# Kernel tuning notes

Measured on AMD Instinct MI355X. Metric: run time of the kernel, lower is better.

The kernel has to match this reference:

```python
import jax, jax.numpy as jnp
import numpy as np

NUM_EXPERTS = 8
TOP_K = 2
D_MODEL = 1024
D_HID = 4096
BATCH, SEQ = 2, 2048


def setup_inputs() -> dict:
    key = jax.random.key(0)
    ks = jax.random.split(key, 5)
    s = 0.02  # param scale
    return {
        "x": jax.random.normal(ks[0], (BATCH, SEQ, D_MODEL), dtype=jnp.float32),
        "Wg": jax.random.normal(ks[1], (D_MODEL, NUM_EXPERTS), dtype=jnp.float32) * s,
        "bg": jnp.zeros((NUM_EXPERTS,), dtype=jnp.float32),
        "W0": jax.random.normal(ks[2], (NUM_EXPERTS, D_MODEL, D_HID), dtype=jnp.float32) * s,
        "b0": jnp.zeros((NUM_EXPERTS, D_HID), dtype=jnp.float32),
        "W1": jax.random.normal(ks[3], (NUM_EXPERTS, D_MODEL, D_HID), dtype=jnp.float32) * s,
        "b1": jnp.zeros((NUM_EXPERTS, D_HID), dtype=jnp.float32),
        "W2": jax.random.normal(ks[4], (NUM_EXPERTS, D_HID, D_MODEL), dtype=jnp.float32) * s,
        "b2": jnp.zeros((NUM_EXPERTS, D_MODEL), dtype=jnp.float32),
    }


def reference(x, Wg, bg, W0, b0, W1, b1, W2, b2):
    n, s, d = x.shape
    # --- routing ---
    gate_logits = x @ Wg + bg                      # [n, s, E]
    top_vals, top_idx = jax.lax.top_k(gate_logits, TOP_K)  # [n, s, K]
    w = jax.nn.softmax(top_vals, axis=-1)          # [n, s, K]
    # combine weights scattered back to dense [n, s, E]
    combine = jnp.sum(jax.nn.one_hot(top_idx, NUM_EXPERTS, dtype=x.dtype) * w[..., None], axis=-2)
    # --- dense expert compute (all experts on all tokens, masked combine) ---
    xf = x.reshape(n * s, d)                       # [T, d]
    h = jnp.einsum('td,edh->eth', xf, W0) + b0[:, None, :]   # [E, T, H]
    g = jax.nn.silu(jnp.einsum('td,edh->eth', xf, W1) + b1[:, None, :])
    y = jnp.einsum('eth,ehd->etd', h * g, W2) + b2[:, None, :]  # [E, T, d]
    out = jnp.einsum('te,etd->td', combine.reshape(n * s, NUM_EXPERTS), y)
    return out.reshape(n, s, d)
```

## Files before the change

### kernel.cpp

```cpp
#include <hip/hip_runtime.h>

#define NTOK 4096
#define DM 1024
#define DH 4096
#define NE 8

typedef __attribute__((ext_vector_type(8))) short bf16x8;
typedef __attribute__((ext_vector_type(4))) float f32x4;
typedef __attribute__((ext_vector_type(8))) unsigned short u16x8;

__device__ __forceinline__ ushort f2bf(float f) {
  union { float f; unsigned u; } v; v.f = f;
  unsigned r = v.u + 0x7fffu + ((v.u >> 16) & 1u);
  return (ushort)(r >> 16);
}

#define GL2LDS(g, l) __builtin_amdgcn_global_load_lds( \
    (__attribute__((address_space(1))) const void*)(g), \
    (__attribute__((address_space(3))) void*)(l), 16, 0, 0)

__global__ __launch_bounds__(256) void gate_kernel(
    const float* __restrict__ x, const float* __restrict__ Wg,
    const float* __restrict__ bg, int* __restrict__ tkE,
    float* __restrict__ tkW, int* __restrict__ gcnt)
{
  const int wave = threadIdx.x >> 6;
  const int lane = threadIdx.x & 63;
  const int t = blockIdx.x * 4 + wave;

  float acc[NE];
#pragma unroll
  for (int e = 0; e < NE; e++) acc[e] = 0.f;

  for (int i = 0; i < DM / 64; i++) {
    int d = i * 64 + lane;
    float xv = x[(long)t * DM + d];
#pragma unroll
    for (int e = 0; e < NE; e++) acc[e] += xv * Wg[d * NE + e];
  }
#pragma unroll
  for (int e = 0; e < NE; e++) {
#pragma unroll
    for (int off = 32; off; off >>= 1) acc[e] += __shfl_xor(acc[e], off, 64);
    acc[e] += bg[e];
  }
  int e0 = 0; float v0 = acc[0];
#pragma unroll
  for (int e = 1; e < NE; e++) if (acc[e] > v0) { v0 = acc[e]; e0 = e; }
  int e1 = -1; float v1 = -3.4e38f;
#pragma unroll
  for (int e = 0; e < NE; e++) if (e != e0 && acc[e] > v1) { v1 = acc[e]; e1 = e; }
  float w0 = 1.f / (1.f + __expf(v1 - v0));
  float w1 = 1.f - w0;
  if (lane == 0) {
    tkE[t] = e0 | (e1 << 8);
    tkW[2 * t] = w0;
    tkW[2 * t + 1] = w1;
    atomicAdd(&gcnt[e0], 1);
    atomicAdd(&gcnt[e1], 1);
  }
}

__global__ void scan_kernel(const int* __restrict__ gcnt, int* __restrict__ offs,
                            int* __restrict__ cursor)
{
  if (threadIdx.x == 0) {
    int o = 0;
    for (int e = 0; e < NE; e++) { offs[e] = o; o += gcnt[e]; cursor[e] = 0; }
    offs[NE] = o;
  }
}

__global__ __launch_bounds__(256) void build_kernel(
    const int* __restrict__ tkE, const float* __restrict__ tkW,
    const int* __restrict__ offs, int* __restrict__ cursor,
    int* __restrict__ rmeta, float* __restrict__ rw)
{
  int t = blockIdx.x * 256 + threadIdx.x;
  int ee = tkE[t];
#pragma unroll
  for (int k = 0; k < 2; k++) {
    int e = (k == 0) ? (ee & 0xff) : (ee >> 8);
    int pos = atomicAdd(&cursor[e], 1);
    int row = offs[e] + pos;
    rmeta[row] = t * 2 + k;
    rw[row] = tkW[t * 2 + k];
  }
}

__global__ __launch_bounds__(256) void gather_kernel(
    const float* __restrict__ x, const int* __restrict__ rmeta,
    ushort* __restrict__ xg)
{
  int row = blockIdx.x;
  int t = rmeta[row] >> 1;
  const float4* src = (const float4*)(x + (long)t * DM);
  float4 v = src[threadIdx.x];
  ushort4 o = { f2bf(v.x), f2bf(v.y), f2bf(v.z), f2bf(v.w) };
  *(ushort4*)(xg + (long)row * DM + threadIdx.x * 4) = o;
}

__global__ __launch_bounds__(256) void transpose_cvt(
    const float* __restrict__ src, ushort* __restrict__ dst,
    int R, int C, long srcE, long dstE)
{
  __shared__ __align__(16) float tile[64][68];
  const int e = blockIdx.z;
  const int r0 = blockIdx.y * 64;
  const int c0 = blockIdx.x * 64;
  const float* s = src + (long)e * srcE;
  ushort* d = dst + (long)e * dstE;
  const int tid = threadIdx.x;
  const int lr = tid >> 4;
  const int lc4 = tid & 15;
#pragma unroll
  for (int p = 0; p < 4; p++) {
    int r = p * 16 + lr;
    float4 v = *(const float4*)&s[(long)(r0 + r) * C + c0 + lc4 * 4];
    *(float4*)&tile[r][lc4 * 4] = v;
  }
  __syncthreads();
  const int oc = tid >> 2;
  const int seg = tid & 3;
  u16x8 o0, o1;
#pragma unroll
  for (int j = 0; j < 8; j++) {
    o0[j] = f2bf(tile[seg * 8 + j][oc]);
    o1[j] = f2bf(tile[32 + seg * 8 + j][oc]);
  }
  ushort* dp = &d[(long)(c0 + oc) * R + r0];
  *(u16x8*)(dp + seg * 8) = o0;
  *(u16x8*)(dp + 32 + seg * 8) = o1;
}

__global__ __launch_bounds__(512, 2) void gemm1_kernel(
    const ushort* __restrict__ xg, const ushort* __restrict__ Wt01,
    const float* __restrict__ b0, const float* __restrict__ b1,
    const int* __restrict__ offs, ushort* __restrict__ aout)
{
  const int flat = blockIdx.x;
  const int xcd = flat & 7;
  const int rest = flat >> 3;
  const int mt = rest & 7;
  const int g2 = rest >> 3;
  const int val = g2 * 8 + xcd;
  const int e = val >> 5;
  const int nt = val & 31;

  const int off_e = offs[e];
  const int cnt = offs[e + 1] - off_e;
  if (mt * 256 >= cnt) return;
  const int nbase = nt * 128;

  __shared__ ushort As[2 * 256 * 64];
  __shared__ ushort Bh[2 * 128 * 64];
  __shared__ ushort Bg[2 * 128 * 64];

  const int tid = threadIdx.x;
  const int lane = tid & 63;
  const int wave = tid >> 6;
  const int wm = wave & 3;
  const int wn = wave >> 2;

  const ushort* Ap = xg + (long)(off_e + mt * 256) * DM;
  const ushort* Bhp = Wt01 + (long)e * (2 * DH) * DM + (long)nbase * DM;
  const ushort* Bgp = Bhp + (long)DH * DM;

  f32x4 acc_h[4][4], acc_g[4][4];
#pragma unroll
  for (int i = 0; i < 4; i++)
#pragma unroll
    for (int j = 0; j < 4; j++) {
      acc_h[i][j] = (f32x4){0.f, 0.f, 0.f, 0.f};
      acc_g[i][j] = (f32x4){0.f, 0.f, 0.f, 0.f};
    }

  auto stage = [&](int cur, int k0) {
#pragma unroll
    for (int s = 0; s < 4; s++) {
      int loff = s * 8192 + tid * 16;
      int row = loff >> 7;
      int sg = ((loff >> 4) & 7) ^ (row & 7);
      GL2LDS(Ap + (long)row * DM + k0 + sg * 8, (char*)As + cur * 32768 + loff);
    }
#pragma unroll
    for (int s = 0; s < 2; s++) {
      int loff = s * 8192 + tid * 16;
      int row = loff >> 7;
      int sg = ((loff >> 4) & 7) ^ (row & 7);
      GL2LDS(Bhp + (long)row * DM + k0 + sg * 8, (char*)Bh + cur * 16384 + loff);
      GL2LDS(Bgp + (long)row * DM + k0 + sg * 8, (char*)Bg + cur * 16384 + loff);
    }
  };

  stage(0, 0);
  stage(1, 64);

  for (int t = 0; t < 16; t++) {
    const int cur = t & 1;
    if (t < 15) asm volatile("s_waitcnt vmcnt(8)" ::: "memory");
    else        asm volatile("s_waitcnt vmcnt(0)" ::: "memory");
    __builtin_amdgcn_s_barrier();
    asm volatile("" ::: "memory");

    const char* Ab  = (const char*)As + cur * 32768;
    const char* Bhb = (const char*)Bh + cur * 16384;
    const char* Bgb = (const char*)Bg + cur * 16384;

    bf16x8 af[4][2];
#pragma unroll
    for (int mi = 0; mi < 4; mi++)
#pragma unroll
      for (int ks = 0; ks < 2; ks++) {
        int row = wm * 64 + mi * 16 + (lane & 15);
        int seg = ks * 4 + (lane >> 4);
        af[mi][ks] = *(const bf16x8*)(Ab + row * 128 + ((seg ^ (row & 7)) << 4));
      }
#pragma unroll
    for (int j = 0; j < 4; j++) {
      bf16x8 bh[2], bg[2];
#pragma unroll
      for (int ks = 0; ks < 2; ks++) {
        int row = wn * 64 + j * 16 + (lane & 15);
        int seg = ks * 4 + (lane >> 4);
        int o = row * 128 + ((seg ^ (row & 7)) << 4);
        bh[ks] = *(const bf16x8*)(Bhb + o);
        bg[ks] = *(const bf16x8*)(Bgb + o);
      }
      __builtin_amdgcn_s_setprio(1);
#pragma unroll
      for (int mi = 0; mi < 4; mi++) {
        acc_h[mi][j] = __builtin_amdgcn_mfma_f32_16x16x32_bf16(af[mi][0], bh[0], acc_h[mi][j], 0, 0, 0);
        acc_h[mi][j] = __builtin_amdgcn_mfma_f32_16x16x32_bf16(af[mi][1], bh[1], acc_h[mi][j], 0, 0, 0);
        acc_g[mi][j] = __builtin_amdgcn_mfma_f32_16x16x32_bf16(af[mi][0], bg[0], acc_g[mi][j], 0, 0, 0);
        acc_g[mi][j] = __builtin_amdgcn_mfma_f32_16x16x32_bf16(af[mi][1], bg[1], acc_g[mi][j], 0, 0, 0);
      }
      __builtin_amdgcn_s_setprio(0);
      __builtin_amdgcn_s_barrier();
    }
    asm volatile("" ::: "memory");
    if (t + 2 < 16) stage(cur, (t + 2) * 64);
  }

#pragma unroll
  for (int j = 0; j < 4; j++) {
    const int col = nbase + wn * 64 + j * 16 + (lane & 15);
    const float bb0 = b0[e * DH + col];
    const float bb1 = b1[e * DH + col];
#pragma unroll
    for (int mi = 0; mi < 4; mi++) {
#pragma unroll
      for (int r = 0; r < 4; r++) {
        int mlocal = mt * 256 + wm * 64 + mi * 16 + (lane >> 4) * 4 + r;
        if (mlocal < cnt) {
          float h = acc_h[mi][j][r] + bb0;
          float g = acc_g[mi][j][r] + bb1;
          float a = h * (g / (1.f + __expf(-g)));
          aout[(long)(off_e + mlocal) * DH + col] = f2bf(a);
        }
      }
    }
  }
}

__global__ __launch_bounds__(512, 2) void gemm2_kernel(
    const ushort* __restrict__ aout, const ushort* __restrict__ W2t,
    const int* __restrict__ offs, const int* __restrict__ rmeta,
    const float* __restrict__ rw, float* __restrict__ ybuf)
{
  const int flat = blockIdx.x;
  const int xcd = flat & 7;
  const int rest = flat >> 3;
  const int mt = rest & 7;
  const int g2 = rest >> 3;
  const int val = g2 * 8 + xcd;
  const int e = val >> 3;
  const int r2 = val & 7;
  const int nt = r2 >> 1;
  const int kc = r2 & 1;

  const int off_e = offs[e];
  const int cnt = offs[e + 1] - off_e;
  if (mt * 256 >= cnt) return;
  const int nbase = nt * 256;
  const int kbase = kc * 2048;

  __shared__ ushort As[2 * 256 * 64];
  __shared__ ushort Bs[2 * 256 * 64];

  const int tid = threadIdx.x;
  const int lane = tid & 63;
  const int wave = tid >> 6;
  const int wm = wave & 1;
  const int wn = wave >> 1;

  const ushort* Ap = aout + (long)(off_e + mt * 256) * DH;
  const ushort* Bp = W2t + (long)e * DM * DH + (long)nbase * DH;

  f32x4 acc[8][4];
#pragma unroll
  for (int i = 0; i < 8; i++)
#pragma unroll
    for (int j = 0; j < 4; j++) acc[i][j] = (f32x4){0.f, 0.f, 0.f, 0.f};

  auto stage = [&](int cur, int k0) {
#pragma unroll
    for (int s = 0; s < 4; s++) {
      int loff = s * 8192 + tid * 16;
      int row = loff >> 7;
      int sg = ((loff >> 4) & 7) ^ (row & 7);
      long gelem = (long)row * DH + k0 + sg * 8;
      GL2LDS(Ap + gelem, (char*)As + cur * 32768 + loff);
      GL2LDS(Bp + gelem, (char*)Bs + cur * 32768 + loff);
    }
  };

  stage(0, kbase);
  stage(1, kbase + 64);

  for (int t = 0; t < 32; t++) {
    const int cur = t & 1;
    if (t < 31) asm volatile("s_waitcnt vmcnt(8)" ::: "memory");
    else        asm volatile("s_waitcnt vmcnt(0)" ::: "memory");
    __builtin_amdgcn_s_barrier();
    asm volatile("" ::: "memory");

    const char* Ab = (const char*)As + cur * 32768;
    const char* Bb = (const char*)Bs + cur * 32768;

    bf16x8 af[8][2];
#pragma unroll
    for (int mi = 0; mi < 8; mi++)
#pragma unroll
      for (int ks = 0; ks < 2; ks++) {
        int row = wm * 128 + mi * 16 + (lane & 15);
        int seg = ks * 4 + (lane >> 4);
        af[mi][ks] = *(const bf16x8*)(Ab + row * 128 + ((seg ^ (row & 7)) << 4));
      }
#pragma unroll
    for (int j = 0; j < 4; j++) {
      bf16x8 bf2[2];
#pragma unroll
      for (int ks = 0; ks < 2; ks++) {
        int row = wn * 64 + j * 16 + (lane & 15);
        int seg = ks * 4 + (lane >> 4);
        bf2[ks] = *(const bf16x8*)(Bb + row * 128 + ((seg ^ (row & 7)) << 4));
      }
      __builtin_amdgcn_s_setprio(1);
#pragma unroll
      for (int mi = 0; mi < 8; mi++) {
        acc[mi][j] = __builtin_amdgcn_mfma_f32_16x16x32_bf16(af[mi][0], bf2[0], acc[mi][j], 0, 0, 0);
        acc[mi][j] = __builtin_amdgcn_mfma_f32_16x16x32_bf16(af[mi][1], bf2[1], acc[mi][j], 0, 0, 0);
      }
      __builtin_amdgcn_s_setprio(0);
      __builtin_amdgcn_s_barrier();
    }
    asm volatile("" ::: "memory");
    if (t + 2 < 32) stage(cur, kbase + (t + 2) * 64);
  }

#pragma unroll
  for (int j = 0; j < 4; j++) {
    const int col = nbase + wn * 64 + j * 16 + (lane & 15);
#pragma unroll
    for (int mi = 0; mi < 8; mi++) {
#pragma unroll
      for (int r = 0; r < 4; r++) {
        int mlocal = mt * 256 + wm * 128 + mi * 16 + (lane >> 4) * 4 + r;
        if (mlocal < cnt) {
          int grow = off_e + mlocal;
          ybuf[((long)kc * 8192 + rmeta[grow]) * DM + col] = rw[grow] * acc[mi][j][r];
        }
      }
    }
  }
}

__global__ __launch_bounds__(256) void combine_kernel(
    const float* __restrict__ ybuf, const int* __restrict__ tkE,
    const float* __restrict__ tkW, const float* __restrict__ b2,
    float* __restrict__ out)
{
  const int t = blockIdx.x;
  const int c = threadIdx.x * 4;
  const int ee = tkE[t];
  const int e0 = ee & 0xff, e1 = ee >> 8;
  const float w0 = tkW[2 * t], w1 = tkW[2 * t + 1];

  float4 acc = {0.f, 0.f, 0.f, 0.f};
#pragma unroll
  for (int kc = 0; kc < 2; kc++) {
#pragma unroll
    for (int k = 0; k < 2; k++) {
      const float4 v = *(const float4*)&ybuf[((long)kc * 8192 + 2 * t + k) * DM + c];
      acc.x += v.x; acc.y += v.y; acc.z += v.z; acc.w += v.w;
    }
  }
  const float4 p0 = *(const float4*)&b2[(long)e0 * DM + c];
  const float4 p1 = *(const float4*)&b2[(long)e1 * DM + c];
  acc.x += w0 * p0.x + w1 * p1.x;
  acc.y += w0 * p0.y + w1 * p1.y;
  acc.z += w0 * p0.z + w1 * p1.z;
  acc.w += w0 * p0.w + w1 * p1.w;
  *(float4*)&out[(long)t * DM + c] = acc;
}

extern "C" void kernel_launch(void* const* d_in, const int* in_sizes, int n_in,
                              void* d_out, int out_size, void* d_ws, size_t ws_size,
                              hipStream_t stream) {
  const float* x  = (const float*)d_in[0];
  const float* Wg = (const float*)d_in[1];
  const float* bg = (const float*)d_in[2];
  const float* W0 = (const float*)d_in[3];
  const float* b0 = (const float*)d_in[4];
  const float* W1 = (const float*)d_in[5];
  const float* b1 = (const float*)d_in[6];
  const float* W2 = (const float*)d_in[7];
  const float* b2 = (const float*)d_in[8];
  float* out = (float*)d_out;

  char* ws = (char*)d_ws;
  ushort* Wt01 = (ushort*)(ws + 0);
  float*  ybuf = (float*)(ws + 0);
  ushort* W2t  = (ushort*)(ws + 134217728);
  ushort* xg   = (ushort*)(ws + 201326592);
  ushort* aout = (ushort*)(ws + 218628096);
  int*    tkE  = (int*)(ws + 287834112);
  float*  tkW  = (float*)(ws + 287850496);
  int*    rmeta= (int*)(ws + 287883264);
  float*  rw   = (float*)(ws + 287916032);
  int*    gcnt = (int*)(ws + 287948800);
  int*    offs = gcnt + 8;
  int*    cursor = gcnt + 20;

  hipMemsetAsync(gcnt, 0, 32, stream);
  gate_kernel<<<NTOK / 4, 256, 0, stream>>>(x, Wg, bg, tkE, tkW, gcnt);
  scan_kernel<<<1, 64, 0, stream>>>(gcnt, offs, cursor);
  build_kernel<<<NTOK / 256, 256, 0, stream>>>(tkE, tkW, offs, cursor, rmeta, rw);
  gather_kernel<<<2 * NTOK, 256, 0, stream>>>(x, rmeta, xg);

  transpose_cvt<<<dim3(64, 16, 8), 256, 0, stream>>>(
      W0, Wt01, 1024, 4096, (long)1024 * 4096, (long)8192 * 1024);
  transpose_cvt<<<dim3(64, 16, 8), 256, 0, stream>>>(
      W1, Wt01 + (long)4096 * 1024, 1024, 4096, (long)1024 * 4096, (long)8192 * 1024);
  transpose_cvt<<<dim3(16, 64, 8), 256, 0, stream>>>(
      W2, W2t, 4096, 1024, (long)4096 * 1024, (long)1024 * 4096);

  gemm1_kernel<<<2048, 512, 0, stream>>>(xg, Wt01, b0, b1, offs, aout);
  gemm2_kernel<<<512, 512, 0, stream>>>(aout, W2t, offs, rmeta, rw, ybuf);
  combine_kernel<<<dim3(NTOK), 256, 0, stream>>>(ybuf, tkE, tkW, b2, out);
}
```

Measured before the change: 1.079 ms.

## Interleave global-to-LDS staging with MFMA sub-steps in both expert GEMMs

Splits the tile staging into separate A-half and B loads and issues them at different j sub-iterations of the inner MFMA loop, rather than all at once after the K-step. B for the next buffer is loaded early and the A halves are loaded into the just-consumed buffer. Wait counts and barriers are moved to match. The goal is to spread memory traffic across the compute phase and hide load latency, at the cost of more barriers and tighter vmcnt and lgkmcnt bookkeeping, which raises the risk of races.

```diff
diff --git a/kernel.cpp b/kernel.cpp
--- a/kernel.cpp
+++ b/kernel.cpp
@@ -8,6 +8,8 @@
 typedef __attribute__((ext_vector_type(8))) short bf16x8;
 typedef __attribute__((ext_vector_type(4))) float f32x4;
 typedef __attribute__((ext_vector_type(8))) unsigned short u16x8;
+
+#define FENCE asm volatile("" ::: "memory")
 
 __device__ __forceinline__ ushort f2bf(float f) {
   union { float f; unsigned u; } v; v.f = f;
@@ -175,14 +177,16 @@
       acc_g[i][j] = (f32x4){0.f, 0.f, 0.f, 0.f};
     }
 
-  auto stage = [&](int cur, int k0) {
-#pragma unroll
-    for (int s = 0; s < 4; s++) {
-      int loff = s * 8192 + tid * 16;
+  auto stageA = [&](int cur, int k0, int half) {
+#pragma unroll
+    for (int s = 0; s < 2; s++) {
+      int loff = (half * 2 + s) * 8192 + tid * 16;
       int row = loff >> 7;
       int sg = ((loff >> 4) & 7) ^ (row & 7);
       GL2LDS(Ap + (long)row * DM + k0 + sg * 8, (char*)As + cur * 32768 + loff);
     }
+  };
+  auto stageB = [&](int cur, int k0) {
 #pragma unroll
     for (int s = 0; s < 2; s++) {
       int loff = s * 8192 + tid * 16;
@@ -193,40 +197,49 @@
     }
   };
 
-  stage(0, 0);
-  stage(1, 64);
+  stageA(0, 0, 0); stageA(0, 0, 1); stageB(0, 0);
+  stageA(1, 64, 0); stageA(1, 64, 1);
+  asm volatile("s_waitcnt vmcnt(4)" ::: "memory");
+  __builtin_amdgcn_s_barrier();
+
+  bf16x8 af[4][2], bh[2], bg[2];
 
   for (int t = 0; t < 16; t++) {
     const int cur = t & 1;
-    if (t < 15) asm volatile("s_waitcnt vmcnt(8)" ::: "memory");
-    else        asm volatile("s_waitcnt vmcnt(0)" ::: "memory");
-    __builtin_amdgcn_s_barrier();
-    asm volatile("" ::: "memory");
-
     const char* Ab  = (const char*)As + cur * 32768;
     const char* Bhb = (const char*)Bh + cur * 16384;
     const char* Bgb = (const char*)Bg + cur * 16384;
 
-    bf16x8 af[4][2];
-#pragma unroll
-    for (int mi = 0; mi < 4; mi++)
-#pragma unroll
-      for (int ks = 0; ks < 2; ks++) {
-        int row = wm * 64 + mi * 16 + (lane & 15);
-        int seg = ks * 4 + (lane >> 4);
-        af[mi][ks] = *(const bf16x8*)(Ab + row * 128 + ((seg ^ (row & 7)) << 4));
-      }
 #pragma unroll
     for (int j = 0; j < 4; j++) {
-      bf16x8 bh[2], bg[2];
-#pragma unroll
-      for (int ks = 0; ks < 2; ks++) {
+      if (j == 0) {
+#pragma unroll
+        for (int mi = 0; mi < 4; mi++)
+#pragma unroll
+          for (int ks = 0; ks < 2; ks++) {
+            int row = wm * 64 + mi * 16 + (lane & 15);
+            int seg = ks * 4 + (lane >> 4);
+            af[mi][ks] = *(const bf16x8*)(Ab + row * 128 + ((seg ^ (row & 7)) << 4));
+          }
+      }
+      {
         int row = wn * 64 + j * 16 + (lane & 15);
-        int seg = ks * 4 + (lane >> 4);
-        int o = row * 128 + ((seg ^ (row & 7)) << 4);
-        bh[ks] = *(const bf16x8*)(Bhb + o);
-        bg[ks] = *(const bf16x8*)(Bgb + o);
-      }
+#pragma unroll
+        for (int ks = 0; ks < 2; ks++) {
+          int seg = ks * 4 + (lane >> 4);
+          int o = row * 128 + ((seg ^ (row & 7)) << 4);
+          bh[ks] = *(const bf16x8*)(Bhb + o);
+          bg[ks] = *(const bf16x8*)(Bgb + o);
+        }
+      }
+      if (j == 0) asm volatile("s_waitcnt lgkmcnt(8)" ::: "memory");
+      if (j == 1 && t + 1 < 16) stageB(cur ^ 1, (t + 1) * 64);
+      if (j == 2 && t + 2 < 16) stageA(cur, (t + 2) * 64, 0);
+      if (j == 3 && t + 2 < 16) stageA(cur, (t + 2) * 64, 1);
+      FENCE;
+      __builtin_amdgcn_s_barrier();
+      asm volatile("s_waitcnt lgkmcnt(0)" ::: "memory");
+      __builtin_amdgcn_sched_barrier(0);
       __builtin_amdgcn_s_setprio(1);
 #pragma unroll
       for (int mi = 0; mi < 4; mi++) {
@@ -236,10 +249,13 @@
         acc_g[mi][j] = __builtin_amdgcn_mfma_f32_16x16x32_bf16(af[mi][1], bg[1], acc_g[mi][j], 0, 0, 0);
       }
       __builtin_amdgcn_s_setprio(0);
+      if (j == 3) {
+        if (t < 14)       asm volatile("s_waitcnt vmcnt(4)" ::: "memory");
+        else if (t == 14) asm volatile("s_waitcnt vmcnt(0)" ::: "memory");
+      }
+      FENCE;
       __builtin_amdgcn_s_barrier();
     }
-    asm volatile("" ::: "memory");
-    if (t + 2 < 16) stage(cur, (t + 2) * 64);
   }
 
 #pragma unroll
@@ -303,49 +319,65 @@
 #pragma unroll
     for (int j = 0; j < 4; j++) acc[i][j] = (f32x4){0.f, 0.f, 0.f, 0.f};
 
-  auto stage = [&](int cur, int k0) {
+  auto stageA = [&](int cur, int k0, int half) {
+#pragma unroll
+    for (int s = 0; s < 2; s++) {
+      int loff = (half * 2 + s) * 8192 + tid * 16;
+      int row = loff >> 7;
+      int sg = ((loff >> 4) & 7) ^ (row & 7);
+      GL2LDS(Ap + (long)row * DH + k0 + sg * 8, (char*)As + cur * 32768 + loff);
+    }
+  };
+  auto stageB = [&](int cur, int k0) {
 #pragma unroll
     for (int s = 0; s < 4; s++) {
       int loff = s * 8192 + tid * 16;
       int row = loff >> 7;
       int sg = ((loff >> 4) & 7) ^ (row & 7);
-      long gelem = (long)row * DH + k0 + sg * 8;
-      GL2LDS(Ap + gelem, (char*)As + cur * 32768 + loff);
-      GL2LDS(Bp + gelem, (char*)Bs + cur * 32768 + loff);
+      GL2LDS(Bp + (long)row * DH + k0 + sg * 8, (char*)Bs + cur * 32768 + loff);
     }
   };
 
-  stage(0, kbase);
-  stage(1, kbase + 64);
+  stageA(0, kbase, 0); stageA(0, kbase, 1); stageB(0, kbase);
+  stageA(1, kbase + 64, 0); stageA(1, kbase + 64, 1);
+  asm volatile("s_waitcnt vmcnt(4)" ::: "memory");
+  __builtin_amdgcn_s_barrier();
+
+  bf16x8 af[8][2], bf2[2];
 
   for (int t = 0; t < 32; t++) {
     const int cur = t & 1;
-    if (t < 31) asm volatile("s_waitcnt vmcnt(8)" ::: "memory");
-    else        asm volatile("s_waitcnt vmcnt(0)" ::: "memory");
-    __builtin_amdgcn_s_barrier();
-    asm volatile("" ::: "memory");
-
     const char* Ab = (const char*)As + cur * 32768;
     const char* Bb = (const char*)Bs + cur * 32768;
 
-    bf16x8 af[8][2];
-#pragma unroll
-    for (int mi = 0; mi < 8; mi++)
-#pragma unroll
-      for (int ks = 0; ks < 2; ks++) {
-        int row = wm * 128 + mi * 16 + (lane & 15);
-        int seg = ks * 4 + (lane >> 4);
-        af[mi][ks] = *(const bf16x8*)(Ab + row * 128 + ((seg ^ (row & 7)) << 4));
-      }
 #pragma unroll
     for (int j = 0; j < 4; j++) {
-      bf16x8 bf2[2];
-#pragma unroll
-      for (int ks = 0; ks < 2; ks++) {
+      if (j == 0) {
+#pragma unroll
+        for (int mi = 0; mi < 8; mi++)
+#pragma unroll
+          for (int ks = 0; ks < 2; ks++) {
+            int row = wm * 128 + mi * 16 + (lane & 15);
+            int seg = ks * 4 + (lane >> 4);
+            af[mi][ks] = *(const bf16x8*)(Ab + row * 128 + ((seg ^ (row & 7)) << 4));
+          }
+      }
+      {
         int row = wn * 64 + j * 16 + (lane & 15);
-        int seg = ks * 4 + (lane >> 4);
-        bf2[ks] = *(const bf16x8*)(Bb + row * 128 + ((seg ^ (row & 7)) << 4));
-      }
+#pragma unroll
+        for (int ks = 0; ks < 2; ks++) {
+          int seg = ks * 4 + (lane >> 4);
+          bf2[ks] = *(const bf16x8*)(Bb + row * 128 + ((seg ^ (row & 7)) << 4));
+        }
+      }
+      if (j == 0) asm volatile("s_waitcnt lgkmcnt(8)" ::: "memory");
+      if (j == 1 && t + 1 < 32) stageB(cur ^ 1, kbase + (t + 1) * 64);
+      if (j == 2 && t + 2 < 32) stageA(cur, kbase + (t + 2) * 64, 0);
+      if (j == 3 && t + 2 < 32) stageA(cur, kbase + (t + 2) * 64, 1);
+      FENCE;
+      __builtin_amdgcn_s_barrier();
+      asm volatile("s_waitcnt lgkmcnt(0)" ::: "memory");
+      __builtin_amdgcn_sched_barrier(0);
       __builtin_amdgcn_s_setprio(1);
 #pragma unroll
       for (int mi = 0; mi < 8; mi++) {
@@ -353,10 +385,13 @@
         acc[mi][j] = __builtin_amdgcn_mfma_f32_16x16x32_bf16(af[mi][1], bf2[1], acc[mi][j], 0, 0, 0);
       }
       __builtin_amdgcn_s_setprio(0);
+      if (j == 3) {
+        if (t < 30)       asm volatile("s_waitcnt vmcnt(4)" ::: "memory");
+        else if (t == 30) asm volatile("s_waitcnt vmcnt(0)" ::: "memory");
+      }
+      FENCE;
       __builtin_amdgcn_s_barrier();
     }
-    asm volatile("" ::: "memory");
-    if (t + 2 < 32) stage(cur, kbase + (t + 2) * 64);
   }
 
 #pragma unroll
```

Result: no change. 1.060 ms (-1.8%).
